# Kernel optimization log

Hardware: AMD Instinct MI355X
Metric: run time of the kernel (lower is better)

The kernel has to match this reference:

```python
import jax, jax.numpy as jnp
import numpy as np

EMBEDDING_DIM = 512
MODEL_DIM = EMBEDDING_DIM
B, S = 32, 2048


def setup_inputs() -> dict:
    key = jax.random.key(0)
    ks = jax.random.split(key, 9)
    d, m = EMBEDDING_DIM, MODEL_DIM
    # xavier_uniform bounds
    def xavier(k, shape):
        fan_out, fan_in = shape
        lim = jnp.sqrt(6.0 / (fan_in + fan_out))
        return jax.random.uniform(k, shape, jnp.float32, -lim, lim)
    return {
        "query": jax.random.normal(ks[0], (B, d), jnp.float32),
        "keys": jax.random.normal(ks[1], (B, S, 2 * d), jnp.float32),
        "key_padding_mask": jax.random.randint(ks[2], (B, S), 0, 2) > 0,
        "Wa_w": xavier(ks[3], (m, d)),
        "Wa_b": jnp.zeros((m,), jnp.float32),
        "Ua_w": xavier(ks[4], (m, 2 * d)),
        "Ua_b": jnp.zeros((m,), jnp.float32),
        "Va_w": xavier(ks[5], (1, m)),
        "Va_b": jnp.zeros((1,), jnp.float32),
    }


def reference(query, keys, key_padding_mask, Wa_w, Wa_b, Ua_w, Ua_b, Va_w, Va_b):
    # Wa(query): [B, M]; Ua(keys): [B, S, M]
    wq = query @ Wa_w.T + Wa_b                      # [B, M]
    uk = jnp.einsum('bse,me->bsm', keys, Ua_w) + Ua_b  # [B, S, M]
    e = jnp.tanh(wq[:, None, :] + uk)               # [B, S, M]
    scores = jnp.einsum('bsm,om->bos', e, Va_w) + Va_b[None, :, None]  # [B, 1, S]
    scores = jnp.where(key_padding_mask[:, None, :], -jnp.inf, scores)
    attn = jax.nn.softmax(scores, axis=-1)          # [B, 1, S]
    context = jnp.einsum('bos,bse->boe', attn, keys)  # [B, 1, 2*EMBEDDING_DIM]
    return context
```

## Files before the change

kernel.cpp:

```cpp
#include <hip/hip_runtime.h>
#include <hip/hip_bf16.h>
#include <cstdint>
#include <cstddef>

#define B_   32
#define S_   2048
#define D_   512
#define K2D  1024
#define M_   512

#define WS_SCORES 0
#define WS_EXPS   65536
#define WS_DENOM  131072
#define WS_WQ     131104
#define WS_FLAG   147488

typedef __attribute__((ext_vector_type(8))) short bf16x8;
typedef __attribute__((ext_vector_type(4))) float f32x4;

__device__ __forceinline__ float tanh_fast(float x) {
    float e = __expf(2.0f * x);
    return 1.0f - 2.0f * __builtin_amdgcn_rcpf(e + 1.0f);
}

union Pack8 { bf16x8 v; __hip_bfloat162 h[4]; };
__device__ __forceinline__ bf16x8 cvt8(float4 a, float4 b) {
    Pack8 p;
    p.h[0] = __float22bfloat162_rn(make_float2(a.x, a.y));
    p.h[1] = __float22bfloat162_rn(make_float2(a.z, a.w));
    p.h[2] = __float22bfloat162_rn(make_float2(b.x, b.y));
    p.h[3] = __float22bfloat162_rn(make_float2(b.z, b.w));
    return p.v;
}

__global__ void k_zero(float* __restrict__ scores, float* __restrict__ denom,
                       float* __restrict__ out) {
    int tid = blockIdx.x * 256 + threadIdx.x;
    if (tid < 65536) scores[tid] = 0.f;
    else if (tid < 65568) denom[tid - 65536] = 0.f;
    if (tid < 32768) out[tid] = 0.f;
}

__global__ void k_flag(const unsigned int* __restrict__ maskw, int* __restrict__ flag) {
    __shared__ int found;
    if (threadIdx.x == 0) found = 0;
    __syncthreads();
    int f = 0;
    for (int i = 0; i < 64; ++i) {
        unsigned v = maskw[threadIdx.x * 64 + i];
        if (v > 1u) f = 1;
    }
    if (f) atomicOr(&found, 1);
    __syncthreads();
    if (threadIdx.x == 0) *flag = found;
}

__global__ __launch_bounds__(256) void k_wq(const float* __restrict__ query,
                                            const float* __restrict__ Wa_w,
                                            const float* __restrict__ Wa_b,
                                            float* __restrict__ wq) {
    int tid = blockIdx.x * 256 + threadIdx.x;
    int b = tid >> 9, m = tid & 511;
    const float4* q = (const float4*)(query + (size_t)b * D_);
    const float4* w = (const float4*)(Wa_w + (size_t)m * D_);
    float acc = 0.f;
    for (int i = 0; i < D_ / 4; ++i) {
        float4 qv = q[i], wv = w[i];
        acc = fmaf(qv.x, wv.x, acc);
        acc = fmaf(qv.y, wv.y, acc);
        acc = fmaf(qv.z, wv.z, acc);
        acc = fmaf(qv.w, wv.w, acc);
    }
    wq[tid] = acc + Wa_b[m];
}

__global__ __launch_bounds__(256, 2) void k_scores(const float* __restrict__ keys,
                                                   const float* __restrict__ Ua_w,
                                                   const float* __restrict__ Ua_b,
                                                   const float* __restrict__ Va_w,
                                                   const float* __restrict__ wq,
                                                   float* __restrict__ scores) {
    __shared__ ushort As[128 * 72];
    __shared__ ushort Bs[128 * 72];

    const int t  = threadIdx.x;
    const int m0 = blockIdx.x * 128;
    const int s0 = blockIdx.y * 128;
    const int b  = blockIdx.z;
    const int wave = t >> 6, lane = t & 63;
    const int q = lane >> 4, r = lane & 15;
    const int sw = (wave >> 1) * 64, mw = (wave & 1) * 64;
    const int rb = t >> 3;
    const int kq = t & 7;

    const float* Ab = keys + ((size_t)b * S_ + s0 + rb) * K2D + kq * 8;
    const float* Bb = Ua_w + ((size_t)(m0 + rb)) * K2D + kq * 8;
    ushort* aw = &As[rb * 72 + kq * 8];
    ushort* bw = &Bs[rb * 72 + kq * 8];

    f32x4 acc[4][4];
#pragma unroll
    for (int i = 0; i < 4; ++i)
#pragma unroll
        for (int j = 0; j < 4; ++j) acc[i][j] = (f32x4){0.f, 0.f, 0.f, 0.f};

    for (int kt = 0; kt < K2D / 64; ++kt) {
        const int ko = kt * 64;
#pragma unroll
        for (int p = 0; p < 4; ++p) {
            const float* sa = Ab + (size_t)(p * 32) * K2D + ko;
            float4 a0 = *(const float4*)sa;
            float4 a1 = *(const float4*)(sa + 4);
            *(bf16x8*)(aw + p * 32 * 72) = cvt8(a0, a1);
            const float* sb = Bb + (size_t)(p * 32) * K2D + ko;
            float4 b0 = *(const float4*)sb;
            float4 b1 = *(const float4*)(sb + 4);
            *(bf16x8*)(bw + p * 32 * 72) = cvt8(b0, b1);
        }
        __syncthreads();
#pragma unroll
        for (int ks = 0; ks < 2; ++ks) {
            bf16x8 af[4], bfr[4];
#pragma unroll
            for (int i = 0; i < 4; ++i)
                af[i] = *(const bf16x8*)&As[(sw + i * 16 + r) * 72 + ks * 32 + q * 8];
#pragma unroll
            for (int j = 0; j < 4; ++j)
                bfr[j] = *(const bf16x8*)&Bs[(mw + j * 16 + r) * 72 + ks * 32 + q * 8];
#pragma unroll
            for (int i = 0; i < 4; ++i)
#pragma unroll
                for (int j = 0; j < 4; ++j)
                    acc[i][j] = __builtin_amdgcn_mfma_f32_16x16x32_bf16(
                        af[i], bfr[j], acc[i][j], 0, 0, 0);
        }
        __syncthreads();
    }

    float vaw[4], wqb[4];
#pragma unroll
    for (int j = 0; j < 4; ++j) {
        int m = m0 + mw + 16 * j + r;
        vaw[j] = Va_w[m];
        wqb[j] = wq[b * M_ + m] + Ua_b[m];
    }
    float* red = (float*)As;
    const int col = (wave & 1) * 16 + r;
#pragma unroll
    for (int i = 0; i < 4; ++i) {
#pragma unroll
        for (int rg = 0; rg < 4; ++rg) {
            int sl = sw + 16 * i + 4 * q + rg;
            float p = 0.f;
#pragma unroll
            for (int j = 0; j < 4; ++j)
                p += vaw[j] * tanh_fast(acc[i][j][rg] + wqb[j]);
            red[sl * 33 + col] = p;
        }
    }
    __syncthreads();
    if (t < 128) {
        float sum = 0.f;
#pragma unroll
        for (int c = 0; c < 32; ++c) sum += red[t * 33 + c];
        atomicAdd(&scores[(size_t)b * S_ + s0 + t], sum);
    }
}

__global__ __launch_bounds__(256) void k_softmax(const float* __restrict__ scores,
                                                 const void* __restrict__ mask,
                                                 const int* __restrict__ flag,
                                                 float* __restrict__ exps,
                                                 float* __restrict__ denom) {
    const int b = blockIdx.x, t = threadIdx.x;
    const bool bytemode = (*flag) != 0;
    const int* mi = (const int*)mask;
    const unsigned char* mb = (const unsigned char*)mask;
    float lsum = 0.f;
#pragma unroll
    for (int i = 0; i < 8; ++i) {
        int s = i * 256 + t;
        size_t idx = (size_t)b * S_ + s;
        bool m = bytemode ? (mb[idx] != 0) : (mi[idx] != 0);
        float v = m ? 0.f : expf(scores[idx]);
        exps[idx] = v;
        lsum += v;
    }
#pragma unroll
    for (int off = 32; off > 0; off >>= 1) lsum += __shfl_down(lsum, off, 64);
    __shared__ float wsum[4];
    if ((t & 63) == 0) wsum[t >> 6] = lsum;
    __syncthreads();
    if (t == 0) denom[b] = wsum[0] + wsum[1] + wsum[2] + wsum[3];
}

__global__ __launch_bounds__(256) void k_context(const float* __restrict__ keys,
                                                 const float* __restrict__ exps,
                                                 const float* __restrict__ denom,
                                                 float* __restrict__ out) {
    __shared__ float w[64];
    const int s0 = blockIdx.x * 64;
    const int b  = blockIdx.y;
    const int t  = threadIdx.x;
    if (t < 64) w[t] = exps[(size_t)b * S_ + s0 + t];
    __syncthreads();
    const float4* kp = (const float4*)(keys + ((size_t)b * S_ + s0) * K2D);
    float4 acc = {0.f, 0.f, 0.f, 0.f};
#pragma unroll 8
    for (int s = 0; s < 64; ++s) {
        float ws = w[s];
        float4 kv = kp[(size_t)s * 256 + t];
        acc.x = fmaf(ws, kv.x, acc.x);
        acc.y = fmaf(ws, kv.y, acc.y);
        acc.z = fmaf(ws, kv.z, acc.z);
        acc.w = fmaf(ws, kv.w, acc.w);
    }
    float inv = 1.0f / denom[b];
    atomicAdd(&out[b * 1024 + t * 4 + 0], acc.x * inv);
    atomicAdd(&out[b * 1024 + t * 4 + 1], acc.y * inv);
    atomicAdd(&out[b * 1024 + t * 4 + 2], acc.z * inv);
    atomicAdd(&out[b * 1024 + t * 4 + 3], acc.w * inv);
}

extern "C" void kernel_launch(void* const* d_in, const int* in_sizes, int n_in,
                              void* d_out, int out_size, void* d_ws, size_t ws_size,
                              hipStream_t stream) {
    const float* query = (const float*)d_in[0];
    const float* keys  = (const float*)d_in[1];
    const void*  mask  = d_in[2];
    const float* Wa_w  = (const float*)d_in[3];
    const float* Wa_b  = (const float*)d_in[4];
    const float* Ua_w  = (const float*)d_in[5];
    const float* Ua_b  = (const float*)d_in[6];
    const float* Va_w  = (const float*)d_in[7];

    float* wsf    = (float*)d_ws;
    float* scores = wsf + WS_SCORES;
    float* exps   = wsf + WS_EXPS;
    float* denom  = wsf + WS_DENOM;
    float* wq     = wsf + WS_WQ;
    int*   flag   = (int*)(wsf + WS_FLAG);
    float* out    = (float*)d_out;

    k_zero<<<257, 256, 0, stream>>>(scores, denom, out);
    k_flag<<<1, 256, 0, stream>>>((const unsigned int*)mask, flag);
    k_wq<<<64, 256, 0, stream>>>(query, Wa_w, Wa_b, wq);
    k_scores<<<dim3(M_ / 128, S_ / 128, B_), 256, 0, stream>>>(keys, Ua_w, Ua_b,
                                                               Va_w, wq, scores);
    k_softmax<<<B_, 256, 0, stream>>>(scores, mask, flag, exps, denom);
    k_context<<<dim3(S_ / 64, B_), 256, 0, stream>>>(keys, exps, denom, out);
}
```

Before: 570.6 us.

## Fuse prep kernels, load MFMA operands directly to registers, merge softmax into context

Merges the zero, flag and wq kernels into one prep kernel, and folds the softmax into the context kernel, which recomputes the per-batch denominator in each block. The score GEMM drops its LDS staging: each wave loads its fp32 fragments straight from global memory into registers, prefetches the next k-step and converts to bf16 in registers. It also remaps blocks so that tiles sharing the same keys rows land on the same XCD. The aim is to cut launch count, LDS traffic and barriers. The cost is redundant global loads across waves, since each keys row is now read by both m-halves, plus redundant softmax work across the 8 context blocks per batch, and the context kernel now has only 256 blocks.

```diff
diff --git a/kernel.cpp b/kernel.cpp
--- a/kernel.cpp
+++ b/kernel.cpp
@@ -10,10 +10,8 @@
 #define M_   512
 
 #define WS_SCORES 0
-#define WS_EXPS   65536
-#define WS_DENOM  131072
-#define WS_WQ     131104
-#define WS_FLAG   147488
+#define WS_WQ     65536
+#define WS_FLAG   81920
 
 typedef __attribute__((ext_vector_type(8))) short bf16x8;
 typedef __attribute__((ext_vector_type(4))) float f32x4;
@@ -33,45 +31,44 @@
     return p.v;
 }
 
-__global__ void k_zero(float* __restrict__ scores, float* __restrict__ denom,
-                       float* __restrict__ out) {
-    int tid = blockIdx.x * 256 + threadIdx.x;
-    if (tid < 65536) scores[tid] = 0.f;
-    else if (tid < 65568) denom[tid - 65536] = 0.f;
-    if (tid < 32768) out[tid] = 0.f;
-}
-
-__global__ void k_flag(const unsigned int* __restrict__ maskw, int* __restrict__ flag) {
-    __shared__ int found;
-    if (threadIdx.x == 0) found = 0;
-    __syncthreads();
-    int f = 0;
-    for (int i = 0; i < 64; ++i) {
-        unsigned v = maskw[threadIdx.x * 64 + i];
-        if (v > 1u) f = 1;
-    }
-    if (f) atomicOr(&found, 1);
-    __syncthreads();
-    if (threadIdx.x == 0) *flag = found;
-}
-
-__global__ __launch_bounds__(256) void k_wq(const float* __restrict__ query,
-                                            const float* __restrict__ Wa_w,
-                                            const float* __restrict__ Wa_b,
-                                            float* __restrict__ wq) {
-    int tid = blockIdx.x * 256 + threadIdx.x;
-    int b = tid >> 9, m = tid & 511;
-    const float4* q = (const float4*)(query + (size_t)b * D_);
-    const float4* w = (const float4*)(Wa_w + (size_t)m * D_);
-    float acc = 0.f;
-    for (int i = 0; i < D_ / 4; ++i) {
-        float4 qv = q[i], wv = w[i];
-        acc = fmaf(qv.x, wv.x, acc);
-        acc = fmaf(qv.y, wv.y, acc);
-        acc = fmaf(qv.z, wv.z, acc);
-        acc = fmaf(qv.w, wv.w, acc);
-    }
-    wq[tid] = acc + Wa_b[m];
+__global__ __launch_bounds__(256) void k_prep(const float* __restrict__ query,
+                                              const float* __restrict__ Wa_w,
+                                              const float* __restrict__ Wa_b,
+                                              const unsigned int* __restrict__ maskw,
+                                              float* __restrict__ scores,
+                                              float* __restrict__ wq,
+                                              float* __restrict__ out,
+                                              int* __restrict__ flag) {
+    const int blk = blockIdx.x, t = threadIdx.x;
+    const int tid = blk * 256 + t;
+    if (blk < 256) {
+        scores[tid] = 0.f;
+        if (tid < 32768) out[tid] = 0.f;
+        if (tid < 16384) {
+            const int b = tid >> 9, m = tid & 511;
+            const float4* q = (const float4*)(query + (size_t)b * D_);
+            const float4* w = (const float4*)(Wa_w + (size_t)m * D_);
+            float acc = 0.f;
+            for (int i = 0; i < D_ / 4; ++i) {
+                float4 qv = q[i], wv = w[i];
+                acc = fmaf(qv.x, wv.x, acc);
+                acc = fmaf(qv.y, wv.y, acc);
+                acc = fmaf(qv.z, wv.z, acc);
+                acc = fmaf(qv.w, wv.w, acc);
+            }
+            wq[tid] = acc + Wa_b[m];
+        }
+    } else {
+        __shared__ int found;
+        if (t == 0) found = 0;
+        __syncthreads();
+        int f = 0;
+        for (int i = 0; i < 64; ++i)
+            if (maskw[t * 64 + i] > 1u) f = 1;
+        if (f) atomicOr(&found, 1);
+        __syncthreads();
+        if (t == 0) *flag = found;
+    }
 }
 
 __global__ __launch_bounds__(256, 2) void k_scores(const float* __restrict__ keys,
@@ -80,23 +77,23 @@
                                                    const float* __restrict__ Va_w,
                                                    const float* __restrict__ wq,
                                                    float* __restrict__ scores) {
-    __shared__ ushort As[128 * 72];
-    __shared__ ushort Bs[128 * 72];
-
-    const int t  = threadIdx.x;
-    const int m0 = blockIdx.x * 128;
-    const int s0 = blockIdx.y * 128;
-    const int b  = blockIdx.z;
+    __shared__ float red[128 * 33];
+
+    const int h    = blockIdx.x;
+    const int xcd  = h & 7, slot = h >> 3;
+    const int mj   = slot & 3;
+    const int grp  = xcd + 8 * (slot >> 2);
+    const int b    = grp >> 4;
+    const int s0   = (grp & 15) * 128;
+    const int m0   = mj * 128;
+
+    const int t = threadIdx.x;
     const int wave = t >> 6, lane = t & 63;
     const int q = lane >> 4, r = lane & 15;
     const int sw = (wave >> 1) * 64, mw = (wave & 1) * 64;
-    const int rb = t >> 3;
-    const int kq = t & 7;
-
-    const float* Ab = keys + ((size_t)b * S_ + s0 + rb) * K2D + kq * 8;
-    const float* Bb = Ua_w + ((size_t)(m0 + rb)) * K2D + kq * 8;
-    ushort* aw = &As[rb * 72 + kq * 8];
-    ushort* bw = &Bs[rb * 72 + kq * 8];
+
+    const float* Abase = keys + ((size_t)b * S_ + s0 + sw + r) * K2D + q * 8;
+    const float* Bbase = Ua_w + ((size_t)(m0 + mw + r)) * K2D + q * 8;
 
     f32x4 acc[4][4];
 #pragma unroll
@@ -104,37 +101,41 @@
 #pragma unroll
         for (int j = 0; j < 4; ++j) acc[i][j] = (f32x4){0.f, 0.f, 0.f, 0.f};
 
-    for (int kt = 0; kt < K2D / 64; ++kt) {
-        const int ko = kt * 64;
-#pragma unroll
-        for (int p = 0; p < 4; ++p) {
-            const float* sa = Ab + (size_t)(p * 32) * K2D + ko;
-            float4 a0 = *(const float4*)sa;
-            float4 a1 = *(const float4*)(sa + 4);
-            *(bf16x8*)(aw + p * 32 * 72) = cvt8(a0, a1);
-            const float* sb = Bb + (size_t)(p * 32) * K2D + ko;
-            float4 b0 = *(const float4*)sb;
-            float4 b1 = *(const float4*)(sb + 4);
-            *(bf16x8*)(bw + p * 32 * 72) = cvt8(b0, b1);
-        }
-        __syncthreads();
+    float4 fa[4][2], fb[4][2];
+#pragma unroll
+    for (int i = 0; i < 4; ++i) {
+        fa[i][0] = *(const float4*)(Abase + i * 16 * K2D);
+        fa[i][1] = *(const float4*)(Abase + i * 16 * K2D + 4);
+        fb[i][0] = *(const float4*)(Bbase + i * 16 * K2D);
+        fb[i][1] = *(const float4*)(Bbase + i * 16 * K2D + 4);
+    }
+
+    for (int kt = 0; kt < 16; ++kt) {
 #pragma unroll
         for (int ks = 0; ks < 2; ++ks) {
-            bf16x8 af[4], bfr[4];
-#pragma unroll
-            for (int i = 0; i < 4; ++i)
-                af[i] = *(const bf16x8*)&As[(sw + i * 16 + r) * 72 + ks * 32 + q * 8];
-#pragma unroll
-            for (int j = 0; j < 4; ++j)
-                bfr[j] = *(const bf16x8*)&Bs[(mw + j * 16 + r) * 72 + ks * 32 + q * 8];
+            bf16x8 af[4], bf[4];
+#pragma unroll
+            for (int i = 0; i < 4; ++i) {
+                af[i] = cvt8(fa[i][0], fa[i][1]);
+                bf[i] = cvt8(fb[i][0], fb[i][1]);
+            }
+            const int nxt = kt * 64 + ks * 32 + 32;
+            if (nxt < K2D) {
+#pragma unroll
+                for (int i = 0; i < 4; ++i) {
+                    fa[i][0] = *(const float4*)(Abase + i * 16 * K2D + nxt);
+                    fa[i][1] = *(const float4*)(Abase + i * 16 * K2D + nxt + 4);
+                    fb[i][0] = *(const float4*)(Bbase + i * 16 * K2D + nxt);
+                    fb[i][1] = *(const float4*)(Bbase + i * 16 * K2D + nxt + 4);
+                }
+            }
 #pragma unroll
             for (int i = 0; i < 4; ++i)
 #pragma unroll
                 for (int j = 0; j < 4; ++j)
                     acc[i][j] = __builtin_amdgcn_mfma_f32_16x16x32_bf16(
-                        af[i], bfr[j], acc[i][j], 0, 0, 0);
+                        af[i], bf[j], acc[i][j], 0, 0, 0);
         }
-        __syncthreads();
     }
 
     float vaw[4], wqb[4];
@@ -144,7 +145,6 @@
         vaw[j] = Va_w[m];
         wqb[j] = wq[b * M_ + m] + Ua_b[m];
     }
-    float* red = (float*)As;
     const int col = (wave & 1) * 16 + r;
 #pragma unroll
     for (int i = 0; i < 4; ++i) {
@@ -167,55 +167,46 @@
     }
 }
 
-__global__ __launch_bounds__(256) void k_softmax(const float* __restrict__ scores,
-                                                 const void* __restrict__ mask,
-                                                 const int* __restrict__ flag,
-                                                 float* __restrict__ exps,
-                                                 float* __restrict__ denom) {
-    const int b = blockIdx.x, t = threadIdx.x;
+__global__ __launch_bounds__(256) void k_ctx(const float* __restrict__ keys,
+                                             const float* __restrict__ scores,
+                                             const void* __restrict__ mask,
+                                             const int* __restrict__ flag,
+                                             float* __restrict__ out) {
+    __shared__ float wbuf[256];
+    __shared__ float wsum_[4];
+    const int c = blockIdx.x, b = blockIdx.y, t = threadIdx.x;
     const bool bytemode = (*flag) != 0;
     const int* mi = (const int*)mask;
     const unsigned char* mb = (const unsigned char*)mask;
+
     float lsum = 0.f;
 #pragma unroll
     for (int i = 0; i < 8; ++i) {
-        int s = i * 256 + t;
-        size_t idx = (size_t)b * S_ + s;
-        bool m = bytemode ? (mb[idx] != 0) : (mi[idx] != 0);
-        float v = m ? 0.f : expf(scores[idx]);
-        exps[idx] = v;
+        const int s = i * 256 + t;
+        const size_t idx = (size_t)b * S_ + s;
+        const bool m = bytemode ? (mb[idx] != 0) : (mi[idx] != 0);
+        const float v = m ? 0.f : expf(scores[idx]);
+        if (i == c) wbuf[t] = v;
         lsum += v;
     }
 #pragma unroll
     for (int off = 32; off > 0; off >>= 1) lsum += __shfl_down(lsum, off, 64);
-    __shared__ float wsum[4];
-    if ((t & 63) == 0) wsum[t >> 6] = lsum;
+    if ((t & 63) == 0) wsum_[t >> 6] = lsum;
     __syncthreads();
-    if (t == 0) denom[b] = wsum[0] + wsum[1] + wsum[2] + wsum[3];
-}
-
-__global__ __launch_bounds__(256) void k_context(const float* __restrict__ keys,
-                                                 const float* __restrict__ exps,
-                                                 const float* __restrict__ denom,
-                                                 float* __restrict__ out) {
-    __shared__ float w[64];
-    const int s0 = blockIdx.x * 64;
-    const int b  = blockIdx.y;
-    const int t  = threadIdx.x;
-    if (t < 64) w[t] = exps[(size_t)b * S_ + s0 + t];
-    __syncthreads();
-    const float4* kp = (const float4*)(keys + ((size_t)b * S_ + s0) * K2D);
+    const float denom = wsum_[0] + wsum_[1] + wsum_[2] + wsum_[3];
+    const float inv = 1.0f / denom;
+
+    const float4* kp = (const float4*)(keys + ((size_t)b * S_ + c * 256) * K2D);
     float4 acc = {0.f, 0.f, 0.f, 0.f};
 #pragma unroll 8
-    for (int s = 0; s < 64; ++s) {
-        float ws = w[s];
-        float4 kv = kp[(size_t)s * 256 + t];
+    for (int s = 0; s < 256; ++s) {
+        const float ws = wbuf[s];
+        const float4 kv = kp[(size_t)s * 256 + t];
         acc.x = fmaf(ws, kv.x, acc.x);
         acc.y = fmaf(ws, kv.y, acc.y);
         acc.z = fmaf(ws, kv.z, acc.z);
         acc.w = fmaf(ws, kv.w, acc.w);
     }
-    float inv = 1.0f / denom[b];
     atomicAdd(&out[b * 1024 + t * 4 + 0], acc.x * inv);
     atomicAdd(&out[b * 1024 + t * 4 + 1], acc.y * inv);
     atomicAdd(&out[b * 1024 + t * 4 + 2], acc.z * inv);
@@ -236,17 +227,13 @@
 
     float* wsf    = (float*)d_ws;
     float* scores = wsf + WS_SCORES;
-    float* exps   = wsf + WS_EXPS;
-    float* denom  = wsf + WS_DENOM;
     float* wq     = wsf + WS_WQ;
     int*   flag   = (int*)(wsf + WS_FLAG);
     float* out    = (float*)d_out;
 
-    k_zero<<<257, 256, 0, stream>>>(scores, denom, out);
-    k_flag<<<1, 256, 0, stream>>>((const unsigned int*)mask, flag);
-    k_wq<<<64, 256, 0, stream>>>(query, Wa_w, Wa_b, wq);
-    k_scores<<<dim3(M_ / 128, S_ / 128, B_), 256, 0, stream>>>(keys, Ua_w, Ua_b,
-                                                               Va_w, wq, scores);
-    k_softmax<<<B_, 256, 0, stream>>>(scores, mask, flag, exps, denom);
-    k_context<<<dim3(S_ / 64, B_), 256, 0, stream>>>(keys, exps, denom, out);
-}
+    k_prep<<<257, 256, 0, stream>>>(query, Wa_w, Wa_b,
+                                    (const unsigned int*)mask,
+                                    scores, wq, out, flag);
+    k_scores<<<2048, 256, 0, stream>>>(keys, Ua_w, Ua_b, Va_w, wq, scores);
+    k_ctx<<<dim3(8, B_), 256, 0, stream>>>(keys, scores, mask, flag, out);
+}
```

Result: slower. 802.0 us (+40.6%).
